# Optimization experiments

Measured on AMD Instinct MI355X. Metric: run time of the kernel, lower is better.

Reference implementation:

```python
import jax, jax.numpy as jnp
import numpy as np
from jax import lax

# dims
B_SZ, H_SZ, W_SZ = 2, 48, 48
D_MODEL = 192
SSM_RATIO = 2.0
D_PROJ = int(SSM_RATIO * D_MODEL)        # 384
C_INNER = 2 * D_PROJ                     # 768 = K * D_IN
K_GRP = 4
D_IN = C_INNER // K_GRP                  # 192 (= d_inner, channel_divide=2)
N_STATE = 16
R_RANK = 12                              # ceil(192/16)


def setup_inputs() -> dict:
    key = jax.random.key(0)
    ks = jax.random.split(key, 12)
    x = jax.random.normal(ks[0], (B_SZ, H_SZ, W_SZ, 2 * D_MODEL), jnp.float32)
    in_proj_w = jax.random.normal(ks[1], (C_INNER, 2 * D_MODEL), jnp.float32) * 0.02
    conv_w = jax.random.normal(ks[2], (C_INNER, 1, 3, 3), jnp.float32) * 0.1
    conv_b = jnp.zeros((C_INNER,), jnp.float32)
    x_proj_weight = jax.random.normal(ks[3], (K_GRP, R_RANK + 2 * N_STATE, D_IN), jnp.float32) * 0.05
    dt_projs_weight = jax.random.normal(ks[4], (K_GRP, D_IN, R_RANK), jnp.float32) * (R_RANK ** -0.5)
    # faithful dt bias init: softplus^{-1}(dt) with dt ~ logU[1e-3, 1e-1]
    dt = jnp.exp(jax.random.uniform(ks[5], (K_GRP, D_IN)) * (np.log(0.1) - np.log(0.001)) + np.log(0.001))
    dt = jnp.clip(dt, 1e-4, None)
    dt_projs_bias = dt + jnp.log(-jnp.expm1(-dt))
    # A_log init: log(arange(1..N)) per channel, K copies merged
    A_logs = jnp.log(jnp.tile(jnp.arange(1, N_STATE + 1, dtype=jnp.float32)[None, :], (K_GRP * D_IN, 1)))
    Ds = jnp.ones((K_GRP * D_IN,), jnp.float32)
    out_norm_w = jnp.ones((C_INNER,), jnp.float32)
    out_norm_b = jnp.zeros((C_INNER,), jnp.float32)
    out_proj_w = jax.random.normal(ks[6], (2 * D_MODEL, C_INNER), jnp.float32) * 0.02
    return dict(x=x, in_proj_w=in_proj_w, conv_w=conv_w, conv_b=conv_b,
                x_proj_weight=x_proj_weight, dt_projs_weight=dt_projs_weight,
                dt_projs_bias=dt_projs_bias, A_logs=A_logs, Ds=Ds,
                out_norm_w=out_norm_w, out_norm_b=out_norm_b, out_proj_w=out_proj_w)


def _ss2d(x, in_proj_w, conv_w, conv_b, x_proj_weight, dt_projs_weight,
          dt_projs_bias, A_logs, Ds, out_norm_w, out_norm_b, out_proj_w):
    B, H, W, _ = x.shape
    C = in_proj_w.shape[0]
    K = x_proj_weight.shape[0]
    d = C // K
    N = A_logs.shape[1]
    R = dt_projs_weight.shape[2]
    L = H * W

    # in_proj (disable_z: no gating split)
    xz = jnp.einsum('bhwc,oc->bhwo', x, in_proj_w)
    xc = xz.transpose(0, 3, 1, 2)  # [B,C,H,W]
    # depthwise 3x3 conv + SiLU
    xc = lax.conv_general_dilated(xc, conv_w, (1, 1), 'SAME', feature_group_count=C)
    xc = xc + conv_b[None, :, None, None]
    xc = xc * jax.nn.sigmoid(xc)

    # CrossScanS: split channels into K groups, each scanned in its own direction
    ch = xc.reshape(B, K, d, H, W)
    f0 = ch[:, 0].reshape(B, d, L)                                        # row-major fwd
    f1 = ch[:, 1].transpose(0, 1, 3, 2).reshape(B, d, L)                  # col-major fwd
    f2 = jnp.flip(ch[:, 2].reshape(B, d, L), -1)                          # row-major rev
    f3 = jnp.flip(ch[:, 3].transpose(0, 1, 3, 2).reshape(B, d, L), -1)    # col-major rev
    xs = jnp.stack([f0, f1, f2, f3], axis=1)  # [B,K,d,L]

    # input-dependent dt/B/C projections
    x_dbl = jnp.einsum('bkdl,kcd->bkcl', xs, x_proj_weight)
    dts, Bs, Cs = jnp.split(x_dbl, [R, R + N], axis=2)  # [B,K,R,L],[B,K,N,L],[B,K,N,L]
    dts = jnp.einsum('bkrl,kdr->bkdl', dts, dt_projs_weight) + dt_projs_bias[None, :, :, None]

    # force_fp32 selective scan with delta_softplus
    u = xs.astype(jnp.float32)
    dts = jax.nn.softplus(dts.astype(jnp.float32))
    Bs = Bs.astype(jnp.float32)
    Cs = Cs.astype(jnp.float32)
    A = -jnp.exp(A_logs.astype(jnp.float32)).reshape(K, d, N)  # [K,d,N]

    def step(h, inp):
        u_t, dt_t, B_t, C_t = inp  # [B,K,d],[B,K,d],[B,K,N],[B,K,N]
        h = h * jnp.exp(dt_t[..., None] * A) + (dt_t * u_t)[..., None] * B_t[:, :, None, :]
        y_t = jnp.einsum('bkdn,bkn->bkd', h, C_t)
        return h, y_t

    inps = (u.transpose(3, 0, 1, 2), dts.transpose(3, 0, 1, 2),
            Bs.transpose(3, 0, 1, 2), Cs.transpose(3, 0, 1, 2))
    h0 = jnp.zeros((B, K, d, N), jnp.float32)
    _, ys = lax.scan(step, h0, inps)          # ys: [L,B,K,d]
    ys = ys.transpose(1, 2, 3, 0)             # [B,K,d,L]
    ys = ys + Ds.astype(jnp.float32).reshape(K, d)[None, :, :, None] * u

    # CrossMergeS: undo each direction, concat channels back
    y0 = ys[:, 0]
    y1 = ys[:, 1].reshape(B, d, W, H).transpose(0, 1, 3, 2).reshape(B, d, L)
    y2 = jnp.flip(ys[:, 2], -1)
    y3 = jnp.flip(ys[:, 3], -1).reshape(B, d, W, H).transpose(0, 1, 3, 2).reshape(B, d, L)
    y = jnp.concatenate([y0, y1, y2, y3], axis=1).reshape(B, C, H, W).transpose(0, 2, 3, 1)

    # out_norm: LayerNorm over channels
    mu = jnp.mean(y, -1, keepdims=True)
    var = jnp.mean(jnp.square(y - mu), -1, keepdims=True)
    y = (y - mu) * lax.rsqrt(var + 1e-5) * out_norm_w + out_norm_b

    out = jnp.einsum('bhwc,oc->bhwo', y.astype(x.dtype), out_proj_w)
    return out


def reference(x, in_proj_w, conv_w, conv_b, x_proj_weight, dt_projs_weight,
              dt_projs_bias, A_logs, Ds, out_norm_w, out_norm_b, out_proj_w):
    return _ss2d(x, in_proj_w, conv_w, conv_b, x_proj_weight, dt_projs_weight,
                 dt_projs_bias, A_logs, Ds, out_norm_w, out_norm_b, out_proj_w)
```

## Files before the change

### kernel.cpp

```cpp
#include <hip/hip_runtime.h>
#include <hip/hip_bf16.h>

#define B_SZ   2
#define H_SZ   48
#define W_SZ   48
#define L_SZ   2304
#define CIN    768
#define KG     4
#define DI     192
#define NS     16
#define RR     12
#define XD     44
#define MTOK   4608
#define CL     16
#define NC     144
#define NXF    (MTOK * 384)
#define NWF    (CIN * 384)

typedef __attribute__((ext_vector_type(8))) short short8;
typedef __attribute__((ext_vector_type(4))) float f32x4;

__device__ inline ushort f2b(float f) {
    uint u = __builtin_bit_cast(uint, f);
    u = (u + 0x7FFF + ((u >> 16) & 1)) >> 16;
    return (ushort)u;
}
__device__ inline float b2f(ushort b) {
    uint u = ((uint)b) << 16;
    return __builtin_bit_cast(float, u);
}
__device__ inline short8 f2b8(float4 a, float4 b) {
    short8 r;
    r[0] = (short)f2b(a.x); r[1] = (short)f2b(a.y);
    r[2] = (short)f2b(a.z); r[3] = (short)f2b(a.w);
    r[4] = (short)f2b(b.x); r[5] = (short)f2b(b.y);
    r[6] = (short)f2b(b.z); r[7] = (short)f2b(b.w);
    return r;
}

__global__ __launch_bounds__(256) void to_bf16_3(
        const float* __restrict__ x, const float* __restrict__ inw,
        const float* __restrict__ outw, ushort* __restrict__ xb,
        ushort* __restrict__ inwb, ushort* __restrict__ outwb) {
    int i4 = (blockIdx.x * 256 + threadIdx.x) * 4;
    const float* src; ushort* dst; int off;
    if (i4 < NXF)             { src = x;    dst = xb;    off = i4; }
    else if (i4 < NXF + NWF)  { src = inw;  dst = inwb;  off = i4 - NXF; }
    else                      { src = outw; dst = outwb; off = i4 - NXF - NWF; }
    float4 v = *(const float4*)&src[off];
    ushort4 u = {f2b(v.x), f2b(v.y), f2b(v.z), f2b(v.w)};
    *(ushort4*)&dst[off] = u;
}

__device__ inline void gridbar(uint* bar, uint nb) {
    __syncthreads();
    if (threadIdx.x == 0) {
        uint g = __hip_atomic_load(&bar[1], __ATOMIC_RELAXED, __HIP_MEMORY_SCOPE_AGENT);
        uint a = __hip_atomic_fetch_add(&bar[0], 1u, __ATOMIC_ACQ_REL, __HIP_MEMORY_SCOPE_AGENT);
        if (a == nb - 1u) {
            __hip_atomic_store(&bar[0], 0u, __ATOMIC_RELAXED, __HIP_MEMORY_SCOPE_AGENT);
            __hip_atomic_store(&bar[1], g + 1u, __ATOMIC_RELEASE, __HIP_MEMORY_SCOPE_AGENT);
        } else {
            while (__hip_atomic_load(&bar[1], __ATOMIC_ACQUIRE, __HIP_MEMORY_SCOPE_AGENT) == g) {
                __builtin_amdgcn_s_sleep(8);
            }
        }
    }
    __syncthreads();
}

template<int TM, int TN, bool ABF, bool BBF, bool CBF>
__global__ __launch_bounds__(256) void gemm_tn(
        const void* __restrict__ Av, const void* __restrict__ Bw,
        void* __restrict__ Cv, int M, int N, int K) {
    __shared__ ushort As[TM][72];
    __shared__ ushort Bs[TN][72];
    constexpr int MF   = TM / 64;
    constexpr int NF   = TN / 16;
    constexpr int ANUM = TM / 32;
    constexpr int BNUM = TN / 32;
    const int tid  = threadIdx.x;
    const int lane = tid & 63;
    const int wave = tid >> 6;
    const int wrow = wave * (MF * 16);
    const int bm = blockIdx.y * TM, bn = blockIdx.x * TN;
    const int frow = lane & 15;
    const int fk   = (lane >> 4) * 8;
    const int orow = (lane >> 4) * 4;

    f32x4 acc[MF][NF] = {};

    for (int k0 = 0; k0 < K; k0 += 64) {
        short8 aval[ANUM];
#pragma unroll
        for (int i = 0; i < ANUM; ++i) {
            int idx = tid + i * 256;
            int row = idx >> 3, q = idx & 7;
            if (ABF) {
                aval[i] = *(const short8*)&((const ushort*)Av)[(size_t)(bm + row) * K + k0 + q * 8];
            } else {
                const float* ap = &((const float*)Av)[(size_t)(bm + row) * K + k0 + q * 8];
                aval[i] = f2b8(*(const float4*)ap, *(const float4*)(ap + 4));
            }
        }
        short8 bval[BNUM];
#pragma unroll
        for (int i = 0; i < BNUM; ++i) {
            int idx = tid + i * 256;
            int row = idx >> 3, q = idx & 7;
            if (BBF) {
                bval[i] = *(const short8*)&((const ushort*)Bw)[(size_t)(bn + row) * K + k0 + q * 8];
            } else {
                const float* bp = &((const float*)Bw)[(size_t)(bn + row) * K + k0 + q * 8];
                bval[i] = f2b8(*(const float4*)bp, *(const float4*)(bp + 4));
            }
        }

        __syncthreads();
#pragma unroll
        for (int i = 0; i < ANUM; ++i) {
            int idx = tid + i * 256;
            *(short8*)&As[idx >> 3][(idx & 7) * 8] = aval[i];
        }
#pragma unroll
        for (int i = 0; i < BNUM; ++i) {
            int idx = tid + i * 256;
            *(short8*)&Bs[idx >> 3][(idx & 7) * 8] = bval[i];
        }
        __syncthreads();

#pragma unroll
        for (int hf = 0; hf < 2; ++hf) {
            short8 af[MF], bf[NF];
#pragma unroll
            for (int mi = 0; mi < MF; ++mi)
                af[mi] = *(const short8*)&As[wrow + mi * 16 + frow][hf * 32 + fk];
#pragma unroll
            for (int ni = 0; ni < NF; ++ni)
                bf[ni] = *(const short8*)&Bs[ni * 16 + frow][hf * 32 + fk];
#pragma unroll
            for (int mi = 0; mi < MF; ++mi)
#pragma unroll
                for (int ni = 0; ni < NF; ++ni)
                    acc[mi][ni] = __builtin_amdgcn_mfma_f32_16x16x32_bf16(
                                      af[mi], bf[ni], acc[mi][ni], 0, 0, 0);
        }
    }

#pragma unroll
    for (int mi = 0; mi < MF; ++mi) {
        int rbase = bm + wrow + mi * 16 + orow;
#pragma unroll
        for (int ni = 0; ni < NF; ++ni) {
            int col = bn + ni * 16 + frow;
#pragma unroll
            for (int r = 0; r < 4; ++r) {
                if (CBF)
                    ((ushort*)Cv)[(size_t)(rbase + r) * N + col] = f2b(acc[mi][ni][r]);
                else
                    ((float*)Cv)[(size_t)(rbase + r) * N + col] = acc[mi][ni][r];
            }
        }
    }
}

__global__ __launch_bounds__(256) void conv_silu_scatter(
        const ushort* __restrict__ xzb, const float* __restrict__ cw,
        const float* __restrict__ cb, ushort* __restrict__ xsb) {
    int g = blockIdx.x * 256 + threadIdx.x;
    int c8 = g % 96;
    int pos = g / 96;
    int w = pos % W_SZ;
    int h = (pos / W_SZ) % H_SZ;
    int b = pos / (W_SZ * H_SZ);
    int c0 = c8 * 8;

    float wt[72];
    const float* cwp = &cw[c0 * 9];
#pragma unroll
    for (int i = 0; i < 18; ++i) {
        float4 v = *(const float4*)(cwp + i * 4);
        wt[i * 4 + 0] = v.x; wt[i * 4 + 1] = v.y;
        wt[i * 4 + 2] = v.z; wt[i * 4 + 3] = v.w;
    }
    float acc[8];
#pragma unroll
    for (int j = 0; j < 8; ++j) acc[j] = cb[c0 + j];

#pragma unroll
    for (int dh = -1; dh <= 1; ++dh) {
        int hh = h + dh;
        if (hh < 0 || hh >= H_SZ) continue;
#pragma unroll
        for (int dw = -1; dw <= 1; ++dw) {
            int ww = w + dw;
            if (ww < 0 || ww >= W_SZ) continue;
            int tap = (dh + 1) * 3 + (dw + 1);
            short8 xv = *(const short8*)&xzb[(size_t)((b * H_SZ + hh) * W_SZ + ww) * CIN + c0];
#pragma unroll
            for (int j = 0; j < 8; ++j)
                acc[j] = fmaf(b2f((ushort)xv[j]), wt[j * 9 + tap], acc[j]);
        }
    }

    float s[8];
#pragma unroll
    for (int j = 0; j < 8; ++j)
        s[j] = acc[j] * __builtin_amdgcn_rcpf(1.f + __expf(-acc[j]));

    int k = c0 / DI, d = c0 % DI;
    int lrow = h * W_SZ + w;
    int lcol = w * H_SZ + h;
    int l;
    if      (k == 0) l = lrow;
    else if (k == 1) l = lcol;
    else if (k == 2) l = L_SZ - 1 - lrow;
    else             l = L_SZ - 1 - lcol;
    float4 lo = {s[0], s[1], s[2], s[3]}, hi = {s[4], s[5], s[6], s[7]};
    *(short8*)&xsb[(size_t)((b * KG + k) * L_SZ + l) * DI + d] = f2b8(lo, hi);
}

__global__ __launch_bounds__(384) void xproj_dt_mfma(
        const ushort* __restrict__ xsb, const float* __restrict__ xpw,
        const float* __restrict__ dtw, const float* __restrict__ dtb,
        float* __restrict__ xdbl, ushort* __restrict__ dts_b) {
    __shared__ ushort Ws[48][200];
    __shared__ ushort Wd[192][40];
    __shared__ ushort dsh[32][40];

    const int tid  = threadIdx.x;
    const int lane = tid & 63;
    const int wave = tid >> 6;
    const int bm = blockIdx.x * 32;
    const int bk = blockIdx.y;
    const int k  = bk & 3;
    const int frow = lane & 15;
    const int fk   = (lane >> 4) * 8;
    const int orow = (lane >> 4) * 4;
    const int rg = wave & 1;
    const int cg = wave >> 1;

#pragma unroll
    for (int i = 0; i < 6; ++i) {
        int idx = tid + i * 384;
        int row = idx / 48, g = idx % 48;
        ushort4 u = {0, 0, 0, 0};
        if (row < XD) {
            float4 v = *(const float4*)&xpw[((size_t)(k * XD) + row) * 192 + g * 4];
            u.x = f2b(v.x); u.y = f2b(v.y); u.z = f2b(v.z); u.w = f2b(v.w);
        }
        *(ushort4*)&Ws[row][g * 4] = u;
    }
#pragma unroll
    for (int i = 0; i < 3; ++i) {
        int idx = tid + i * 384;
        if (idx < 960) {
            float4 z = {0.f, 0.f, 0.f, 0.f};
            *(float4*)&Wd[idx / 5][(idx % 5) * 8] = z;
        } else if (idx < 1120) {
            int j = idx - 960;
            float4 z = {0.f, 0.f, 0.f, 0.f};
            *(float4*)&dsh[j / 5][(j % 5) * 8] = z;
        }
    }
    __syncthreads();

#pragma unroll
    for (int i = 0; i < 6; ++i) {
        int idx = tid + i * 384;
        int row = idx / RR, c = idx % RR;
        Wd[row][c] = f2b(dtw[((size_t)(k * DI) + row) * RR + c]);
    }

    f32x4 acc1 = {};
    const ushort* arow = &xsb[(size_t)(bk * L_SZ + bm + rg * 16 + frow) * DI];
#pragma unroll
    for (int k0 = 0; k0 < 192; k0 += 32) {
        short8 af = *(const short8*)&arow[k0 + fk];
        short8 bv = *(const short8*)&Ws[cg * 16 + frow][k0 + fk];
        acc1 = __builtin_amdgcn_mfma_f32_16x16x32_bf16(af, bv, acc1, 0, 0, 0);
    }

    {
        int col = cg * 16 + frow;
#pragma unroll
        for (int r = 0; r < 4; ++r) {
            float v = acc1[r];
            int row = rg * 16 + orow + r;
            if (col >= RR && col < XD)
                xdbl[(size_t)(bk * L_SZ + bm + row) * XD + col] = v;
            if (cg == 0 && col < RR)
                dsh[row][col] = f2b(v);
        }
    }
    __syncthreads();

#pragma unroll
    for (int t = 0; t < 2; ++t) {
        int d = (wave * 2 + t) * 16 + frow;
        short8 bv = *(const short8*)&Wd[d][fk];
        float bias = dtb[k * DI + d];
#pragma unroll
        for (int rg2 = 0; rg2 < 2; ++rg2) {
            short8 af2 = *(const short8*)&dsh[rg2 * 16 + frow][fk];
            f32x4 a2 = {};
            a2 = __builtin_amdgcn_mfma_f32_16x16x32_bf16(af2, bv, a2, 0, 0, 0);
#pragma unroll
            for (int r = 0; r < 4; ++r) {
                float a = a2[r] + bias;
                float sp = fmaxf(a, 0.f) + __logf(1.f + __expf(-fabsf(a)));
                dts_b[(size_t)(bk * L_SZ + bm + rg2 * 16 + orow + r) * DI + d] = f2b(sp);
            }
        }
    }
}

__global__ __launch_bounds__(192, 4) void scan_fused(
        const ushort* __restrict__ dts_b, const ushort* __restrict__ xsb,
        const float* __restrict__ xdbl, const float* __restrict__ A_logs,
        float* __restrict__ Ebuf, float* __restrict__ Sbuf,
        float* __restrict__ Pbuf, float* __restrict__ Hstart,
        const float* __restrict__ Ds, ushort* __restrict__ ypre_b,
        const float* __restrict__ lnw, const float* __restrict__ lnb,
        ushort* __restrict__ ynrm_b, uint* __restrict__ bar) {
    const int blk = blockIdx.x;
    const int bk = blk / NC, ch = blk % NC;
    const int d = threadIdx.x, k = bk % KG, b = bk / KG;
    const int l0 = ch * CL;

    __shared__ float bsh[CL][NS];
    __shared__ float csh[CL][NS];
    __shared__ float red[2][3];
    for (int t = threadIdx.x; t < CL * NS; t += 192) {
        int l = t / NS, n = t % NS;
        const float* row = &xdbl[(size_t)(bk * L_SZ + l0 + l) * XD];
        bsh[l][n] = row[RR + n];
        csh[l][n] = row[RR + NS + n];
    }
    __syncthreads();

    {
        float Aa[NS], S[NS];
        const float* ar = &A_logs[(size_t)(k * DI + d) * NS];
        bool fast = true;
#pragma unroll
        for (int n = 0; n < NS; ++n) {
            Aa[n] = -__expf(ar[n]);
            S[n] = 0.f;
            fast = fast && (fabsf(Aa[n] + (float)(n + 1)) < 1e-4f * (n + 1));
        }
        float* sp = &Sbuf[(size_t)((bk * NC + ch) * DI + d) * NS];
        if (fast) {
            float P = 1.f;
#pragma unroll
            for (int l = 0; l < CL; ++l) {
                float dt = b2f(dts_b[(size_t)(bk * L_SZ + l0 + l) * DI + d]);
                float u  = b2f(xsb [(size_t)(bk * L_SZ + l0 + l) * DI + d]);
                float du = dt * u;
                float4 b0 = *(const float4*)&bsh[l][0];
                float4 b1 = *(const float4*)&bsh[l][4];
                float4 b2 = *(const float4*)&bsh[l][8];
                float4 b3 = *(const float4*)&bsh[l][12];
                float Bv[NS] = {b0.x,b0.y,b0.z,b0.w, b1.x,b1.y,b1.z,b1.w,
                                b2.x,b2.y,b2.z,b2.w, b3.x,b3.y,b3.z,b3.w};
                float e1 = __expf(-dt);
                P *= e1;
                float e = e1;
                S[0] = fmaf(S[0], e, du * Bv[0]);
#pragma unroll
                for (int n = 1; n < NS; ++n) {
                    e *= e1;
                    S[n] = fmaf(S[n], e, du * Bv[n]);
                }
            }
            Pbuf[(size_t)(bk * NC + ch) * DI + d] = P;
#pragma unroll
            for (int q = 0; q < 4; ++q) {
                float4 v = {S[q*4], S[q*4+1], S[q*4+2], S[q*4+3]};
                *(float4*)&sp[q * 4] = v;
            }
        } else {
            float E[NS];
#pragma unroll
            for (int n = 0; n < NS; ++n) E[n] = 1.f;
#pragma unroll 8
            for (int l = 0; l < CL; ++l) {
                float dt = b2f(dts_b[(size_t)(bk * L_SZ + l0 + l) * DI + d]);
                float u  = b2f(xsb [(size_t)(bk * L_SZ + l0 + l) * DI + d]);
                float du = dt * u;
                float4 b0 = *(const float4*)&bsh[l][0];
                float4 b1 = *(const float4*)&bsh[l][4];
                float4 b2 = *(const float4*)&bsh[l][8];
                float4 b3 = *(const float4*)&bsh[l][12];
                float Bv[NS] = {b0.x,b0.y,b0.z,b0.w, b1.x,b1.y,b1.z,b1.w,
                                b2.x,b2.y,b2.z,b2.w, b3.x,b3.y,b3.z,b3.w};
#pragma unroll
                for (int n = 0; n < NS; ++n) {
                    float e = __expf(dt * Aa[n]);
                    E[n] *= e;
                    S[n] = fmaf(S[n], e, du * Bv[n]);
                }
            }
            Pbuf[(size_t)(bk * NC + ch) * DI + d] = -1.f;
            float* ep = &Ebuf[(size_t)((bk * NC + ch) * DI + d) * NS];
#pragma unroll
            for (int q = 0; q < 4; ++q) {
                float4 ve = {E[q*4], E[q*4+1], E[q*4+2], E[q*4+3]};
                float4 vs = {S[q*4], S[q*4+1], S[q*4+2], S[q*4+3]};
                *(float4*)&ep[q * 4] = ve;
                *(float4*)&sp[q * 4] = vs;
            }
        }
    }

    gridbar(bar, gridDim.x);

    {
        constexpr int P = 8;
        int t = blk * 192 + threadIdx.x;
        if (t < 8 * DI * 4) {
            int bkB = t / (DI * 4);
            int dn = (t % (DI * 4)) * 4;
            int dB = dn >> 4;
            int n0 = dn & 15;
            const size_t stride = (size_t)DI * NS;
            size_t off = (size_t)(bkB * NC) * stride + dn;
            const float* pb = &Pbuf[(size_t)(bkB * NC) * DI + dB];

            float4 h = {0.f, 0.f, 0.f, 0.f};
            bool fastu = (pb[0] >= 0.f);

            if (fastu) {
                float  pA[P], pB2[P];
                float4 sA[P], sB[P];
                size_t offL = off;
                int    cP   = 0;
#pragma unroll
                for (int j = 0; j < P; ++j) {
                    pA[j] = pb[(size_t)(cP + j) * DI];
                    sA[j] = *(const float4*)&Sbuf[offL + (size_t)j * stride];
                }
                offL += (size_t)P * stride; cP += P;

                for (int c = 0; c < NC; c += 2 * P) {
#pragma unroll
                    for (int j = 0; j < P; ++j) {
                        pB2[j] = pb[(size_t)(cP + j) * DI];
                        sB[j] = *(const float4*)&Sbuf[offL + (size_t)j * stride];
                    }
                    offL += (size_t)P * stride; cP += P;

#pragma unroll
                    for (int j = 0; j < P; ++j) {
                        *(float4*)&Hstart[off + (size_t)j * stride] = h;
                        float Pv = pA[j];
                        float P2 = Pv * Pv, P3 = P2 * Pv;
                        float P4 = P2 * P2, P8 = P4 * P4;
                        float base = Pv * ((n0 & 4) ? P4 : 1.f) * ((n0 & 8) ? P8 : 1.f);
                        h.x = fmaf(base,      h.x, sA[j].x);
                        h.y = fmaf(base * Pv, h.y, sA[j].y);
                        h.z = fmaf(base * P2, h.z, sA[j].z);
                        h.w = fmaf(base * P3, h.w, sA[j].w);
                    }
                    off += (size_t)P * stride;

                    if (c + 2 * P < NC) {
#pragma unroll
                        for (int j = 0; j < P; ++j) {
                            pA[j] = pb[(size_t)(cP + j) * DI];
                            sA[j] = *(const float4*)&Sbuf[offL + (size_t)j * stride];
                        }
                    }
                    offL += (size_t)P * stride; cP += P;

#pragma unroll
                    for (int j = 0; j < P; ++j) {
                        *(float4*)&Hstart[off + (size_t)j * stride] = h;
                        float Pv = pB2[j];
                        float P2 = Pv * Pv, P3 = P2 * Pv;
                        float P4 = P2 * P2, P8 = P4 * P4;
                        float base = Pv * ((n0 & 4) ? P4 : 1.f) * ((n0 & 8) ? P8 : 1.f);
                        h.x = fmaf(base,      h.x, sB[j].x);
                        h.y = fmaf(base * Pv, h.y, sB[j].y);
                        h.z = fmaf(base * P2, h.z, sB[j].z);
                        h.w = fmaf(base * P3, h.w, sB[j].w);
                    }
                    off += (size_t)P * stride;
                }
            } else {
                float4 eA[P], sA[P], eB[P], sB[P];
                size_t offL = off;
#pragma unroll
                for (int j = 0; j < P; ++j) {
                    eA[j] = *(const float4*)&Ebuf[offL + (size_t)j * stride];
                    sA[j] = *(const float4*)&Sbuf[offL + (size_t)j * stride];
                }
                offL += (size_t)P * stride;

                for (int c = 0; c < NC; c += 2 * P) {
#pragma unroll
                    for (int j = 0; j < P; ++j) {
                        eB[j] = *(const float4*)&Ebuf[offL + (size_t)j * stride];
                        sB[j] = *(const float4*)&Sbuf[offL + (size_t)j * stride];
                    }
                    offL += (size_t)P * stride;

#pragma unroll
                    for (int j = 0; j < P; ++j) {
                        *(float4*)&Hstart[off + (size_t)j * stride] = h;
                        h.x = fmaf(eA[j].x, h.x, sA[j].x);
                        h.y = fmaf(eA[j].y, h.y, sA[j].y);
                        h.z = fmaf(eA[j].z, h.z, sA[j].z);
                        h.w = fmaf(eA[j].w, h.w, sA[j].w);
                    }
                    off += (size_t)P * stride;

                    if (c + 2 * P < NC) {
#pragma unroll
                        for (int j = 0; j < P; ++j) {
                            eA[j] = *(const float4*)&Ebuf[offL + (size_t)j * stride];
                            sA[j] = *(const float4*)&Sbuf[offL + (size_t)j * stride];
                        }
                    }
                    offL += (size_t)P * stride;

#pragma unroll
                    for (int j = 0; j < P; ++j) {
                        *(float4*)&Hstart[off + (size_t)j * stride] = h;
                        h.x = fmaf(eB[j].x, h.x, sB[j].x);
                        h.y = fmaf(eB[j].y, h.y, sB[j].y);
                        h.z = fmaf(eB[j].z, h.z, sB[j].z);
                        h.w = fmaf(eB[j].w, h.w, sB[j].w);
                    }
                    off += (size_t)P * stride;
                }
            }
        }
    }

    gridbar(bar, gridDim.x);

    {
        float Aa[NS], h[NS];
        const float* ar = &A_logs[(size_t)(k * DI + d) * NS];
        const float* hp = &Hstart[(size_t)((bk * NC + ch) * DI + d) * NS];
        bool fast = true;
#pragma unroll
        for (int n = 0; n < NS; ++n) {
            Aa[n] = -__expf(ar[n]);
            h[n] = hp[n];
            fast = fast && (fabsf(Aa[n] + (float)(n + 1)) < 1e-4f * (n + 1));
        }
        float Dd = Ds[k * DI + d];

#pragma unroll 8
        for (int l = 0; l < CL; ++l) {
            float dt = b2f(dts_b[(size_t)(bk * L_SZ + l0 + l) * DI + d]);
            float u  = b2f(xsb [(size_t)(bk * L_SZ + l0 + l) * DI + d]);
            float du = dt * u;
            float4 b0 = *(const float4*)&bsh[l][0];
            float4 b1 = *(const float4*)&bsh[l][4];
            float4 b2 = *(const float4*)&bsh[l][8];
            float4 b3 = *(const float4*)&bsh[l][12];
            float Bv[NS] = {b0.x,b0.y,b0.z,b0.w, b1.x,b1.y,b1.z,b1.w,
                            b2.x,b2.y,b2.z,b2.w, b3.x,b3.y,b3.z,b3.w};
            float4 c0 = *(const float4*)&csh[l][0];
            float4 c1 = *(const float4*)&csh[l][4];
            float4 c2 = *(const float4*)&csh[l][8];
            float4 c3 = *(const float4*)&csh[l][12];
            float Cv[NS] = {c0.x,c0.y,c0.z,c0.w, c1.x,c1.y,c1.z,c1.w,
                            c2.x,c2.y,c2.z,c2.w, c3.x,c3.y,c3.z,c3.w};
            float p[NS];
            if (fast) {
                float e1 = __expf(-dt);
                float e = e1;
                h[0] = fmaf(h[0], e, du * Bv[0]);
                p[0] = h[0] * Cv[0];
#pragma unroll
                for (int n = 1; n < NS; ++n) {
                    e *= e1;
                    h[n] = fmaf(h[n], e, du * Bv[n]);
                    p[n] = h[n] * Cv[n];
                }
            } else {
#pragma unroll
                for (int n = 0; n < NS; ++n) {
                    float e = __expf(dt * Aa[n]);
                    h[n] = fmaf(h[n], e, du * Bv[n]);
                    p[n] = h[n] * Cv[n];
                }
            }
#pragma unroll
            for (int s = 8; s >= 1; s >>= 1)
#pragma unroll
                for (int n = 0; n < 8; ++n)
                    if (n < s) p[n] = p[n] + p[n + s];
            float y = fmaf(Dd, u, p[0]);

            int lg = l0 + l;
            int pos;
            if      (k == 0) pos = lg;
            else if (k == 1) pos = (lg % H_SZ) * W_SZ + (lg / H_SZ);
            else if (k == 2) pos = L_SZ - 1 - lg;
            else { int j = L_SZ - 1 - lg; pos = (j % H_SZ) * W_SZ + (j / H_SZ); }
            ypre_b[(size_t)(b * L_SZ + pos) * CIN + k * DI + d] = f2b(y);
        }
    }

    gridbar(bar, gridDim.x);

    {
        int lane = threadIdx.x & 63, wv = threadIdx.x >> 6;
        int i4 = threadIdx.x * 4;
        float4 w4 = *(const float4*)&lnw[i4];
        float4 g4 = *(const float4*)&lnb[i4];
        for (int j = 0; j < 4; ++j) {
            int tok = blk * 4 + j;
            ushort4 rv = *(const ushort4*)&ypre_b[(size_t)tok * CIN + i4];
            float v0 = b2f(rv.x), v1 = b2f(rv.y), v2 = b2f(rv.z), v3 = b2f(rv.w);
            float s1 = v0 + v1 + v2 + v3;
            float s2 = v0*v0 + v1*v1 + v2*v2 + v3*v3;
#pragma unroll
            for (int off = 32; off >= 1; off >>= 1) {
                s1 += __shfl_xor(s1, off, 64);
                s2 += __shfl_xor(s2, off, 64);
            }
            if (lane == 0) { red[0][wv] = s1; red[1][wv] = s2; }
            __syncthreads();
            float ts1 = red[0][0] + red[0][1] + red[0][2];
            float ts2 = red[1][0] + red[1][1] + red[1][2];
            float mu = ts1 * (1.f / CIN);
            float rstd = rsqrtf(ts2 * (1.f / CIN) - mu * mu + 1e-5f);
            ushort4 o;
            o.x = f2b((v0 - mu) * rstd * w4.x + g4.x);
            o.y = f2b((v1 - mu) * rstd * w4.y + g4.y);
            o.z = f2b((v2 - mu) * rstd * w4.z + g4.z);
            o.w = f2b((v3 - mu) * rstd * w4.w + g4.w);
            *(ushort4*)&ynrm_b[(size_t)tok * CIN + i4] = o;
            __syncthreads();
        }
    }
}

__global__ __launch_bounds__(192) void scan_passA(
        const ushort* __restrict__ dts_b, const ushort* __restrict__ xsb,
        const float* __restrict__ xdbl, const float* __restrict__ A_logs,
        float* __restrict__ Ebuf, float* __restrict__ Sbuf,
        float* __restrict__ Pbuf) {
    int blk = blockIdx.x;
    int bk = blk / NC, ch = blk % NC;
    int d = threadIdx.x, k = bk % KG;
    int l0 = ch * CL;

    __shared__ float bsh[CL][NS];
    for (int t = threadIdx.x; t < CL * NS; t += 192) {
        int l = t / NS, n = t % NS;
        bsh[l][n] = xdbl[(size_t)(bk * L_SZ + l0 + l) * XD + RR + n];
    }
    __syncthreads();

    float Aa[NS], S[NS];
    const float* ar = &A_logs[(size_t)(k * DI + d) * NS];
    bool fast = true;
#pragma unroll
    for (int n = 0; n < NS; ++n) {
        Aa[n] = -__expf(ar[n]);
        S[n] = 0.f;
        fast = fast && (fabsf(Aa[n] + (float)(n + 1)) < 1e-4f * (n + 1));
    }

    float* sp = &Sbuf[(size_t)((bk * NC + ch) * DI + d) * NS];
    if (fast) {
        float P = 1.f;
#pragma unroll
        for (int l = 0; l < CL; ++l) {
            float dt = b2f(dts_b[(size_t)(bk * L_SZ + l0 + l) * DI + d]);
            float u  = b2f(xsb [(size_t)(bk * L_SZ + l0 + l) * DI + d]);
            float du = dt * u;
            float4 b0 = *(const float4*)&bsh[l][0];
            float4 b1 = *(const float4*)&bsh[l][4];
            float4 b2 = *(const float4*)&bsh[l][8];
            float4 b3 = *(const float4*)&bsh[l][12];
            float Bv[NS] = {b0.x,b0.y,b0.z,b0.w, b1.x,b1.y,b1.z,b1.w,
                            b2.x,b2.y,b2.z,b2.w, b3.x,b3.y,b3.z,b3.w};
            float e1 = __expf(-dt);
            P *= e1;
            float e = e1;
            S[0] = fmaf(S[0], e, du * Bv[0]);
#pragma unroll
            for (int n = 1; n < NS; ++n) {
                e *= e1;
                S[n] = fmaf(S[n], e, du * Bv[n]);
            }
        }
        Pbuf[(size_t)(bk * NC + ch) * DI + d] = P;
#pragma unroll
        for (int q = 0; q < 4; ++q) {
            float4 v = {S[q*4], S[q*4+1], S[q*4+2], S[q*4+3]};
            *(float4*)&sp[q * 4] = v;
        }
    } else {
        float E[NS];
#pragma unroll
        for (int n = 0; n < NS; ++n) E[n] = 1.f;
#pragma unroll 8
        for (int l = 0; l < CL; ++l) {
            float dt = b2f(dts_b[(size_t)(bk * L_SZ + l0 + l) * DI + d]);
            float u  = b2f(xsb [(size_t)(bk * L_SZ + l0 + l) * DI + d]);
            float du = dt * u;
            float4 b0 = *(const float4*)&bsh[l][0];
            float4 b1 = *(const float4*)&bsh[l][4];
            float4 b2 = *(const float4*)&bsh[l][8];
            float4 b3 = *(const float4*)&bsh[l][12];
            float Bv[NS] = {b0.x,b0.y,b0.z,b0.w, b1.x,b1.y,b1.z,b1.w,
                            b2.x,b2.y,b2.z,b2.w, b3.x,b3.y,b3.z,b3.w};
#pragma unroll
            for (int n = 0; n < NS; ++n) {
                float e = __expf(dt * Aa[n]);
                E[n] *= e;
                S[n] = fmaf(S[n], e, du * Bv[n]);
            }
        }
        Pbuf[(size_t)(bk * NC + ch) * DI + d] = -1.f;
        float* ep = &Ebuf[(size_t)((bk * NC + ch) * DI + d) * NS];
#pragma unroll
        for (int q = 0; q < 4; ++q) {
            float4 ve = {E[q*4], E[q*4+1], E[q*4+2], E[q*4+3]};
            float4 vs = {S[q*4], S[q*4+1], S[q*4+2], S[q*4+3]};
            *(float4*)&ep[q * 4] = ve;
            *(float4*)&sp[q * 4] = vs;
        }
    }
}

__global__ __launch_bounds__(64) void scan_passB(
        const float* __restrict__ Ebuf, const float* __restrict__ Sbuf,
        const float* __restrict__ Pbuf, float* __restrict__ Hstart) {
    constexpr int P = 8;
    int t = blockIdx.x * 64 + threadIdx.x;
    int bk = t / (DI * 4);
    int dn = (t % (DI * 4)) * 4;
    int d  = dn >> 4;
    int n0 = dn & 15;
    const size_t stride = (size_t)DI * NS;
    size_t off  = (size_t)(bk * NC) * stride + dn;
    const float* pb = &Pbuf[(size_t)(bk * NC) * DI + d];

    float4 h = {0.f, 0.f, 0.f, 0.f};
    bool fastu = (pb[0] >= 0.f);

    if (fastu) {
        float  pA[P], pB[P];
        float4 sA[P], sB[P];
        size_t offL = off;
        int    cP   = 0;
#pragma unroll
        for (int j = 0; j < P; ++j) {
            pA[j] = pb[(size_t)(cP + j) * DI];
            sA[j] = *(const float4*)&Sbuf[offL + (size_t)j * stride];
        }
        offL += (size_t)P * stride; cP += P;

        for (int c = 0; c < NC; c += 2 * P) {
#pragma unroll
            for (int j = 0; j < P; ++j) {
                pB[j] = pb[(size_t)(cP + j) * DI];
                sB[j] = *(const float4*)&Sbuf[offL + (size_t)j * stride];
            }
            offL += (size_t)P * stride; cP += P;

#pragma unroll
            for (int j = 0; j < P; ++j) {
                *(float4*)&Hstart[off + (size_t)j * stride] = h;
                float Pv = pA[j];
                float P2 = Pv * Pv, P3 = P2 * Pv;
                float P4 = P2 * P2, P8 = P4 * P4;
                float base = Pv * ((n0 & 4) ? P4 : 1.f) * ((n0 & 8) ? P8 : 1.f);
                h.x = fmaf(base,      h.x, sA[j].x);
                h.y = fmaf(base * Pv, h.y, sA[j].y);
                h.z = fmaf(base * P2, h.z, sA[j].z);
                h.w = fmaf(base * P3, h.w, sA[j].w);
            }
            off += (size_t)P * stride;

            if (c + 2 * P < NC) {
#pragma unroll
                for (int j = 0; j < P; ++j) {
                    pA[j] = pb[(size_t)(cP + j) * DI];
                    sA[j] = *(const float4*)&Sbuf[offL + (size_t)j * stride];
                }
            }
            offL += (size_t)P * stride; cP += P;

#pragma unroll
            for (int j = 0; j < P; ++j) {
                *(float4*)&Hstart[off + (size_t)j * stride] = h;
                float Pv = pB[j];
                float P2 = Pv * Pv, P3 = P2 * Pv;
                float P4 = P2 * P2, P8 = P4 * P4;
                float base = Pv * ((n0 & 4) ? P4 : 1.f) * ((n0 & 8) ? P8 : 1.f);
                h.x = fmaf(base,      h.x, sB[j].x);
                h.y = fmaf(base * Pv, h.y, sB[j].y);
                h.z = fmaf(base * P2, h.z, sB[j].z);
                h.w = fmaf(base * P3, h.w, sB[j].w);
            }
            off += (size_t)P * stride;
        }
    } else {
        float4 eA[P], sA[P], eB[P], sB[P];
        size_t offL = off;
#pragma unroll
        for (int j = 0; j < P; ++j) {
            eA[j] = *(const float4*)&Ebuf[offL + (size_t)j * stride];
            sA[j] = *(const float4*)&Sbuf[offL + (size_t)j * stride];
        }
        offL += (size_t)P * stride;

        for (int c = 0; c < NC; c += 2 * P) {
#pragma unroll
            for (int j = 0; j < P; ++j) {
                eB[j] = *(const float4*)&Ebuf[offL + (size_t)j * stride];
                sB[j] = *(const float4*)&Sbuf[offL + (size_t)j * stride];
            }
            offL += (size_t)P * stride;

#pragma unroll
            for (int j = 0; j < P; ++j) {
                *(float4*)&Hstart[off + (size_t)j * stride] = h;
                h.x = fmaf(eA[j].x, h.x, sA[j].x);
                h.y = fmaf(eA[j].y, h.y, sA[j].y);
                h.z = fmaf(eA[j].z, h.z, sA[j].z);
                h.w = fmaf(eA[j].w, h.w, sA[j].w);
            }
            off += (size_t)P * stride;

            if (c + 2 * P < NC) {
#pragma unroll
                for (int j = 0; j < P; ++j) {
                    eA[j] = *(const float4*)&Ebuf[offL + (size_t)j * stride];
                    sA[j] = *(const float4*)&Sbuf[offL + (size_t)j * stride];
                }
            }
            offL += (size_t)P * stride;

#pragma unroll
            for (int j = 0; j < P; ++j) {
                *(float4*)&Hstart[off + (size_t)j * stride] = h;
                h.x = fmaf(eB[j].x, h.x, sB[j].x);
                h.y = fmaf(eB[j].y, h.y, sB[j].y);
                h.z = fmaf(eB[j].z, h.z, sB[j].z);
                h.w = fmaf(eB[j].w, h.w, sB[j].w);
            }
            off += (size_t)P * stride;
        }
    }
}

__global__ __launch_bounds__(192) void scan_passC(
        const ushort* __restrict__ dts_b, const ushort* __restrict__ xsb,
        const float* __restrict__ xdbl, const float* __restrict__ A_logs,
        const float* __restrict__ Hstart, const float* __restrict__ Ds,
        ushort* __restrict__ ypre_b) {
    int blk = blockIdx.x;
    int bk = blk / NC, ch = blk % NC;
    int d = threadIdx.x, k = bk % KG, b = bk / KG;
    int l0 = ch * CL;

    __shared__ float bsh[CL][NS];
    __shared__ float csh[CL][NS];
    for (int t = threadIdx.x; t < CL * NS; t += 192) {
        int l = t / NS, n = t % NS;
        const float* row = &xdbl[(size_t)(bk * L_SZ + l0 + l) * XD];
        bsh[l][n] = row[RR + n];
        csh[l][n] = row[RR + NS + n];
    }
    __syncthreads();

    float Aa[NS], h[NS];
    const float* ar = &A_logs[(size_t)(k * DI + d) * NS];
    const float* hp = &Hstart[(size_t)((bk * NC + ch) * DI + d) * NS];
    bool fast = true;
#pragma unroll
    for (int n = 0; n < NS; ++n) {
        Aa[n] = -__expf(ar[n]);
        h[n] = hp[n];
        fast = fast && (fabsf(Aa[n] + (float)(n + 1)) < 1e-4f * (n + 1));
    }
    float Dd = Ds[k * DI + d];

#pragma unroll 8
    for (int l = 0; l < CL; ++l) {
        float dt = b2f(dts_b[(size_t)(bk * L_SZ + l0 + l) * DI + d]);
        float u  = b2f(xsb [(size_t)(bk * L_SZ + l0 + l) * DI + d]);
        float du = dt * u;
        float4 b0 = *(const float4*)&bsh[l][0];
        float4 b1 = *(const float4*)&bsh[l][4];
        float4 b2 = *(const float4*)&bsh[l][8];
        float4 b3 = *(const float4*)&bsh[l][12];
        float Bv[NS] = {b0.x,b0.y,b0.z,b0.w, b1.x,b1.y,b1.z,b1.w,
                        b2.x,b2.y,b2.z,b2.w, b3.x,b3.y,b3.z,b3.w};
        float4 c0 = *(const float4*)&csh[l][0];
        float4 c1 = *(const float4*)&csh[l][4];
        float4 c2 = *(const float4*)&csh[l][8];
        float4 c3 = *(const float4*)&csh[l][12];
        float Cv[NS] = {c0.x,c0.y,c0.z,c0.w, c1.x,c1.y,c1.z,c1.w,
                        c2.x,c2.y,c2.z,c2.w, c3.x,c3.y,c3.z,c3.w};
        float p[NS];
        if (fast) {
            float e1 = __expf(-dt);
            float e = e1;
            h[0] = fmaf(h[0], e, du * Bv[0]);
            p[0] = h[0] * Cv[0];
#pragma unroll
            for (int n = 1; n < NS; ++n) {
                e *= e1;
                h[n] = fmaf(h[n], e, du * Bv[n]);
                p[n] = h[n] * Cv[n];
            }
        } else {
#pragma unroll
            for (int n = 0; n < NS; ++n) {
                float e = __expf(dt * Aa[n]);
                h[n] = fmaf(h[n], e, du * Bv[n]);
                p[n] = h[n] * Cv[n];
            }
        }
#pragma unroll
        for (int s = 8; s >= 1; s >>= 1)
#pragma unroll
            for (int n = 0; n < 8; ++n)
                if (n < s) p[n] = p[n] + p[n + s];
        float y = fmaf(Dd, u, p[0]);

        int lg = l0 + l;
        int pos;
        if      (k == 0) pos = lg;
        else if (k == 1) pos = (lg % H_SZ) * W_SZ + (lg / H_SZ);
        else if (k == 2) pos = L_SZ - 1 - lg;
        else { int j = L_SZ - 1 - lg; pos = (j % H_SZ) * W_SZ + (j / H_SZ); }
        ypre_b[(size_t)(b * L_SZ + pos) * CIN + k * DI + d] = f2b(y);
    }
}

__global__ __launch_bounds__(256) void layernorm_bf16(
        const ushort* __restrict__ y, ushort* __restrict__ yb,
        const float* __restrict__ w, const float* __restrict__ bg) {
    int wave = threadIdx.x >> 6, lane = threadIdx.x & 63;
    int tok = blockIdx.x * 4 + wave;
    const ushort* row = &y[(size_t)tok * CIN];
    ushort* rowo = &yb[(size_t)tok * CIN];
    float v[12];
    float s = 0.f;
#pragma unroll
    for (int i = 0; i < 12; ++i) { v[i] = b2f(row[lane + i * 64]); s += v[i]; }
#pragma unroll
    for (int off = 32; off >= 1; off >>= 1) s += __shfl_xor(s, off, 64);
    float mu = s * (1.f / CIN);
    float s2 = 0.f;
#pragma unroll
    for (int i = 0; i < 12; ++i) { float t = v[i] - mu; s2 += t * t; }
#pragma unroll
    for (int off = 32; off >= 1; off >>= 1) s2 += __shfl_xor(s2, off, 64);
    float rstd = rsqrtf(s2 * (1.f / CIN) + 1e-5f);
#pragma unroll
    for (int i = 0; i < 12; ++i)
        rowo[lane + i * 64] =
            f2b((v[i] - mu) * rstd * w[lane + i * 64] + bg[lane + i * 64]);
}

extern "C" void kernel_launch(void* const* d_in, const int* in_sizes, int n_in,
                              void* d_out, int out_size, void* d_ws, size_t ws_size,
                              hipStream_t stream) {
    const float* x    = (const float*)d_in[0];
    const float* inw  = (const float*)d_in[1];
    const float* cw   = (const float*)d_in[2];
    const float* cb   = (const float*)d_in[3];
    const float* xpw  = (const float*)d_in[4];
    const float* dtw  = (const float*)d_in[5];
    const float* dtb  = (const float*)d_in[6];
    const float* alog = (const float*)d_in[7];
    const float* Dsp  = (const float*)d_in[8];
    const float* lnw  = (const float*)d_in[9];
    const float* lnb  = (const float*)d_in[10];
    const float* outw = (const float*)d_in[11];
    float* out = (float*)d_out;

    float* ws = (float*)d_ws;
    const size_t SZ_BIG = (size_t)MTOK * CIN;
    const size_t SCAN_SL = (size_t)8 * NC * DI * NS;
    float* xz    = ws;
    float* xsbf  = xz  + SZ_BIG;
    float* dts   = xsbf + SZ_BIG / 2;
    float* xdbl  = dts + SZ_BIG;
    float* Ebuf  = xdbl + (size_t)8 * L_SZ * XD;
    float* Sbuf  = Ebuf + SCAN_SL;
    float* Hst   = Sbuf + SCAN_SL;
    float* Pbuf  = Hst + SCAN_SL;
    ushort* xb   = (ushort*)(Pbuf + (size_t)8 * NC * DI);
    ushort* inwb = xb + NXF;
    ushort* outwb= inwb + NWF;
    uint*  bar   = (uint*)(outwb + NWF);
    ushort* xzb    = (ushort*)xz;
    ushort* xsb    = (ushort*)xsbf;
    ushort* dtsb   = (ushort*)dts;
    ushort* ypre_b = (ushort*)xz;
    ushort* ynrm_b = (ushort*)dts;

    to_bf16_3<<<(NXF + 2 * NWF) / 1024, 256, 0, stream>>>(x, inw, outw, xb, inwb, outwb);
    gemm_tn<64, 64, true, true, true><<<dim3(CIN / 64, MTOK / 64), 256, 0, stream>>>(
        xb, inwb, xzb, MTOK, CIN, 384);
    conv_silu_scatter<<<(B_SZ * H_SZ * W_SZ * 96) / 256, 256, 0, stream>>>(xzb, cw, cb, xsb);
    xproj_dt_mfma<<<dim3(L_SZ / 32, 8), 384, 0, stream>>>(xsb, xpw, dtw, dtb, xdbl, dtsb);

    int maxb = 0;
    hipError_t oe = hipOccupancyMaxActiveBlocksPerMultiprocessor(
        &maxb, scan_fused, 192, 0);
    if (oe == hipSuccess && maxb * 256 >= 8 * NC) {
        hipMemsetAsync(bar, 0, 2 * sizeof(uint), stream);
        scan_fused<<<8 * NC, 192, 0, stream>>>(
            dtsb, xsb, xdbl, alog, Ebuf, Sbuf, Pbuf, Hst, Dsp, ypre_b,
            lnw, lnb, ynrm_b, bar);
    } else {
        scan_passA<<<8 * NC, 192, 0, stream>>>(dtsb, xsb, xdbl, alog, Ebuf, Sbuf, Pbuf);
        scan_passB<<<(8 * DI * 4) / 64, 64, 0, stream>>>(Ebuf, Sbuf, Pbuf, Hst);
        scan_passC<<<8 * NC, 192, 0, stream>>>(dtsb, xsb, xdbl, alog, Hst, Dsp, ypre_b);
        layernorm_bf16<<<MTOK / 4, 256, 0, stream>>>(ypre_b, ynrm_b, lnw, lnb);
    }
    gemm_tn<64, 32, true, true, false><<<dim3(384 / 32, MTOK / 64), 256, 0, stream>>>(
        ynrm_b, outwb, out, MTOK, 384, CIN);
}
```

Baseline: 177.1 us.

## Fuse bf16 conversion into in_proj GEMM and out_proj into persistent scan

Merges the fp32-to-bf16 conversion kernel with the in_proj GEMM using a grid-wide barrier, and appends the out_proj GEMM to the persistent scan_fused kernel after another grid barrier, tiling it 48x32 per block. This removes two kernel launches and their inter-kernel gaps. In exchange it relies on all 864 GEMM blocks being co-resident (checked only as at least 4 blocks per CU), adds shared memory to the scan kernel that may lower its occupancy, and uses small output tiles for the out_proj.

```diff
diff --git a/kernel.cpp b/kernel.cpp
--- a/kernel.cpp
+++ b/kernel.cpp
@@ -38,6 +38,97 @@
     return r;
 }
 
+__device__ inline void gridbar(uint* bar, uint nb) {
+    __syncthreads();
+    if (threadIdx.x == 0) {
+        uint g = __hip_atomic_load(&bar[1], __ATOMIC_RELAXED, __HIP_MEMORY_SCOPE_AGENT);
+        uint a = __hip_atomic_fetch_add(&bar[0], 1u, __ATOMIC_ACQ_REL, __HIP_MEMORY_SCOPE_AGENT);
+        if (a == nb - 1u) {
+            __hip_atomic_store(&bar[0], 0u, __ATOMIC_RELAXED, __HIP_MEMORY_SCOPE_AGENT);
+            __hip_atomic_store(&bar[1], g + 1u, __ATOMIC_RELEASE, __HIP_MEMORY_SCOPE_AGENT);
+        } else {
+            while (__hip_atomic_load(&bar[1], __ATOMIC_ACQUIRE, __HIP_MEMORY_SCOPE_AGENT) == g) {
+                __builtin_amdgcn_s_sleep(8);
+            }
+        }
+    }
+    __syncthreads();
+}
+
+__global__ __launch_bounds__(256) void gemm1_fused(
+        const float* __restrict__ x, const float* __restrict__ inw,
+        const float* __restrict__ outw, ushort* __restrict__ xb,
+        ushort* __restrict__ inwb, ushort* __restrict__ outwb,
+        ushort* __restrict__ Cv, uint* __restrict__ bar) {
+    constexpr int N = CIN, K = 384;
+    __shared__ ushort As[64][72];
+    __shared__ ushort Bs[64][72];
+    const int tid  = threadIdx.x;
+    const int flatb = blockIdx.y * gridDim.x + blockIdx.x;
+
+    for (int u = flatb * 256 + tid; u < (NXF + 2 * NWF) / 4; u += 864 * 256) {
+        int i4 = u * 4;
+        const float* src; ushort* dst; int off;
+        if (i4 < NXF)            { src = x;    dst = xb;    off = i4; }
+        else if (i4 < NXF + NWF) { src = inw;  dst = inwb;  off = i4 - NXF; }
+        else                     { src = outw; dst = outwb; off = i4 - NXF - NWF; }
+        float4 v = *(const float4*)&src[off];
+        ushort4 uu = {f2b(v.x), f2b(v.y), f2b(v.z), f2b(v.w)};
+        *(ushort4*)&dst[off] = uu;
+    }
+    gridbar(bar, 864);
+
+    const int lane = tid & 63;
+    const int wave = tid >> 6;
+    const int wrow = wave * 16;
+    const int bm = blockIdx.y * 64, bn = blockIdx.x * 64;
+    const int frow = lane & 15;
+    const int fk   = (lane >> 4) * 8;
+    const int orow = (lane >> 4) * 4;
+
+    f32x4 acc[4] = {};
+
+    for (int k0 = 0; k0 < K; k0 += 64) {
+        short8 aval[2], bval[2];
+#pragma unroll
+        for (int i = 0; i < 2; ++i) {
+            int idx = tid + i * 256;
+            int row = idx >> 3, q = idx & 7;
+            aval[i] = *(const short8*)&xb[(size_t)(bm + row) * K + k0 + q * 8];
+            bval[i] = *(const short8*)&inwb[(size_t)(bn + row) * K + k0 + q * 8];
+        }
+        __syncthreads();
+#pragma unroll
+        for (int i = 0; i < 2; ++i) {
+            int idx = tid + i * 256;
+            *(short8*)&As[idx >> 3][(idx & 7) * 8] = aval[i];
+            *(short8*)&Bs[idx >> 3][(idx & 7) * 8] = bval[i];
+        }
+        __syncthreads();
+
+#pragma unroll
+        for (int hf = 0; hf < 2; ++hf) {
+            short8 af = *(const short8*)&As[wrow + frow][hf * 32 + fk];
+            short8 bf[4];
+#pragma unroll
+            for (int ni = 0; ni < 4; ++ni)
+                bf[ni] = *(const short8*)&Bs[ni * 16 + frow][hf * 32 + fk];
+#pragma unroll
+            for (int ni = 0; ni < 4; ++ni)
+                acc[ni] = __builtin_amdgcn_mfma_f32_16x16x32_bf16(af, bf[ni], acc[ni], 0, 0, 0);
+        }
+    }
+
+    int rbase = bm + wrow + orow;
+#pragma unroll
+    for (int ni = 0; ni < 4; ++ni) {
+        int col = bn + ni * 16 + frow;
+#pragma unroll
+        for (int r = 0; r < 4; ++r)
+            Cv[(size_t)(rbase + r) * N + col] = f2b(acc[ni][r]);
+    }
+}
+
 __global__ __launch_bounds__(256) void to_bf16_3(
         const float* __restrict__ x, const float* __restrict__ inw,
         const float* __restrict__ outw, ushort* __restrict__ xb,
@@ -52,26 +143,9 @@
     *(ushort4*)&dst[off] = u;
 }
 
-__device__ inline void gridbar(uint* bar, uint nb) {
-    __syncthreads();
-    if (threadIdx.x == 0) {
-        uint g = __hip_atomic_load(&bar[1], __ATOMIC_RELAXED, __HIP_MEMORY_SCOPE_AGENT);
-        uint a = __hip_atomic_fetch_add(&bar[0], 1u, __ATOMIC_ACQ_REL, __HIP_MEMORY_SCOPE_AGENT);
-        if (a == nb - 1u) {
-            __hip_atomic_store(&bar[0], 0u, __ATOMIC_RELAXED, __HIP_MEMORY_SCOPE_AGENT);
-            __hip_atomic_store(&bar[1], g + 1u, __ATOMIC_RELEASE, __HIP_MEMORY_SCOPE_AGENT);
-        } else {
-            while (__hip_atomic_load(&bar[1], __ATOMIC_ACQUIRE, __HIP_MEMORY_SCOPE_AGENT) == g) {
-                __builtin_amdgcn_s_sleep(8);
-            }
-        }
-    }
-    __syncthreads();
-}
-
-template<int TM, int TN, bool ABF, bool BBF, bool CBF>
+template<int TM, int TN, bool CBF>
 __global__ __launch_bounds__(256) void gemm_tn(
-        const void* __restrict__ Av, const void* __restrict__ Bw,
+        const ushort* __restrict__ Av, const ushort* __restrict__ Bw,
         void* __restrict__ Cv, int M, int N, int K) {
     __shared__ ushort As[TM][72];
     __shared__ ushort Bs[TN][72];
@@ -91,31 +165,17 @@
     f32x4 acc[MF][NF] = {};
 
     for (int k0 = 0; k0 < K; k0 += 64) {
-        short8 aval[ANUM];
+        short8 aval[ANUM], bval[BNUM];
 #pragma unroll
         for (int i = 0; i < ANUM; ++i) {
             int idx = tid + i * 256;
-            int row = idx >> 3, q = idx & 7;
-            if (ABF) {
-                aval[i] = *(const short8*)&((const ushort*)Av)[(size_t)(bm + row) * K + k0 + q * 8];
-            } else {
-                const float* ap = &((const float*)Av)[(size_t)(bm + row) * K + k0 + q * 8];
-                aval[i] = f2b8(*(const float4*)ap, *(const float4*)(ap + 4));
-            }
-        }
-        short8 bval[BNUM];
+            aval[i] = *(const short8*)&Av[(size_t)(bm + (idx >> 3)) * K + k0 + (idx & 7) * 8];
+        }
 #pragma unroll
         for (int i = 0; i < BNUM; ++i) {
             int idx = tid + i * 256;
-            int row = idx >> 3, q = idx & 7;
-            if (BBF) {
-                bval[i] = *(const short8*)&((const ushort*)Bw)[(size_t)(bn + row) * K + k0 + q * 8];
-            } else {
-                const float* bp = &((const float*)Bw)[(size_t)(bn + row) * K + k0 + q * 8];
-                bval[i] = f2b8(*(const float4*)bp, *(const float4*)(bp + 4));
-            }
-        }
-
+            bval[i] = *(const short8*)&Bw[(size_t)(bn + (idx >> 3)) * K + k0 + (idx & 7) * 8];
+        }
         __syncthreads();
 #pragma unroll
         for (int i = 0; i < ANUM; ++i) {
@@ -322,7 +382,8 @@
         float* __restrict__ Pbuf, float* __restrict__ Hstart,
         const float* __restrict__ Ds, ushort* __restrict__ ypre_b,
         const float* __restrict__ lnw, const float* __restrict__ lnb,
-        ushort* __restrict__ ynrm_b, uint* __restrict__ bar) {
+        ushort* __restrict__ ynrm_b, const ushort* __restrict__ outwb,
+        float* __restrict__ out, uint* __restrict__ bar) {
     const int blk = blockIdx.x;
     const int bk = blk / NC, ch = blk % NC;
     const int d = threadIdx.x, k = bk % KG, b = bk / KG;
@@ -331,6 +392,8 @@
     __shared__ float bsh[CL][NS];
     __shared__ float csh[CL][NS];
     __shared__ float red[2][3];
+    __shared__ ushort As2[48][72];
+    __shared__ ushort Bs2[32][72];
     for (int t = threadIdx.x; t < CL * NS; t += 192) {
         int l = t / NS, n = t % NS;
         const float* row = &xdbl[(size_t)(bk * L_SZ + l0 + l) * XD];
@@ -640,6 +703,65 @@
             __syncthreads();
         }
     }
+
+    gridbar(bar, gridDim.x);
+
+    {
+        const int em = blk / 12, en = blk % 12;
+        const int bm2 = em * 48, bn2 = en * 32;
+        const int lane2 = threadIdx.x & 63;
+        const int wv = threadIdx.x >> 6;
+        const int frow2 = lane2 & 15;
+        const int fk2   = (lane2 >> 4) * 8;
+        const int orow2 = (lane2 >> 4) * 4;
+        f32x4 acc[2] = {};
+
+        for (int k0 = 0; k0 < CIN; k0 += 64) {
+            short8 aval[2];
+#pragma unroll
+            for (int i = 0; i < 2; ++i) {
+                int idx = threadIdx.x + i * 192;
+                aval[i] = *(const short8*)&ynrm_b[(size_t)(bm2 + (idx >> 3)) * CIN + k0 + (idx & 7) * 8];
+            }
+            short8 bval0 = *(const short8*)&outwb[(size_t)(bn2 + (threadIdx.x >> 3)) * CIN + k0 + (threadIdx.x & 7) * 8];
+            short8 bval1;
+            if (threadIdx.x < 64) {
+                int idx = threadIdx.x + 192;
+                bval1 = *(const short8*)&outwb[(size_t)(bn2 + (idx >> 3)) * CIN + k0 + (idx & 7) * 8];
+            }
+            __syncthreads();
+#pragma unroll
+            for (int i = 0; i < 2; ++i) {
+                int idx = threadIdx.x + i * 192;
+                *(short8*)&As2[idx >> 3][(idx & 7) * 8] = aval[i];
+            }
+            *(short8*)&Bs2[threadIdx.x >> 3][(threadIdx.x & 7) * 8] = bval0;
+            if (threadIdx.x < 64) {
+                int idx = threadIdx.x + 192;
+                *(short8*)&Bs2[idx >> 3][(idx & 7) * 8] = bval1;
+            }
+            __syncthreads();
+
+#pragma unroll
+            for (int hf = 0; hf < 2; ++hf) {
+                short8 af = *(const short8*)&As2[wv * 16 + frow2][hf * 32 + fk2];
+#pragma unroll
+                for (int ni = 0; ni < 2; ++ni) {
+                    short8 bf = *(const short8*)&Bs2[ni * 16 + frow2][hf * 32 + fk2];
+                    acc[ni] = __builtin_amdgcn_mfma_f32_16x16x32_bf16(af, bf, acc[ni], 0, 0, 0);
+                }
+            }
+        }
+
+        int rbase = bm2 + wv * 16 + orow2;
+#pragma unroll
+        for (int ni = 0; ni < 2; ++ni) {
+            int col = bn2 + ni * 16 + frow2;
+#pragma unroll
+            for (int r = 0; r < 4; ++r)
+                out[(size_t)(rbase + r) * 384 + col] = acc[ni][r];
+        }
+    }
 }
 
 __global__ __launch_bounds__(192) void scan_passA(
@@ -1006,26 +1128,35 @@
     ushort* ypre_b = (ushort*)xz;
     ushort* ynrm_b = (ushort*)dts;
 
-    to_bf16_3<<<(NXF + 2 * NWF) / 1024, 256, 0, stream>>>(x, inw, outw, xb, inwb, outwb);
-    gemm_tn<64, 64, true, true, true><<<dim3(CIN / 64, MTOK / 64), 256, 0, stream>>>(
-        xb, inwb, xzb, MTOK, CIN, 384);
+    int maxb1 = 0, maxbS = 0;
+    hipError_t e1 = hipOccupancyMaxActiveBlocksPerMultiprocessor(&maxb1, gemm1_fused, 256, 0);
+    hipError_t eS = hipOccupancyMaxActiveBlocksPerMultiprocessor(&maxbS, scan_fused, 192, 0);
+    bool f1 = (e1 == hipSuccess && maxb1 >= 4);
+    bool fS = (eS == hipSuccess && maxbS * 256 >= 8 * NC);
+
+    hipMemsetAsync(bar, 0, 4 * sizeof(uint), stream);
+
+    if (f1) {
+        gemm1_fused<<<dim3(CIN / 64, MTOK / 64), 256, 0, stream>>>(
+            x, inw, outw, xb, inwb, outwb, xzb, bar + 2);
+    } else {
+        to_bf16_3<<<(NXF + 2 * NWF) / 1024, 256, 0, stream>>>(x, inw, outw, xb, inwb, outwb);
+        gemm_tn<64, 64, true><<<dim3(CIN / 64, MTOK / 64), 256, 0, stream>>>(
+            xb, inwb, xzb, MTOK, CIN, 384);
+    }
     conv_silu_scatter<<<(B_SZ * H_SZ * W_SZ * 96) / 256, 256, 0, stream>>>(xzb, cw, cb, xsb);
     xproj_dt_mfma<<<dim3(L_SZ / 32, 8), 384, 0, stream>>>(xsb, xpw, dtw, dtb, xdbl, dtsb);
 
-    int maxb = 0;
-    hipError_t oe = hipOccupancyMaxActiveBlocksPerMultiprocessor(
-        &maxb, scan_fused, 192, 0);
-    if (oe == hipSuccess && maxb * 256 >= 8 * NC) {
-        hipMemsetAsync(bar, 0, 2 * sizeof(uint), stream);
+    if (fS) {
         scan_fused<<<8 * NC, 192, 0, stream>>>(
             dtsb, xsb, xdbl, alog, Ebuf, Sbuf, Pbuf, Hst, Dsp, ypre_b,
-            lnw, lnb, ynrm_b, bar);
+            lnw, lnb, ynrm_b, outwb, out, bar);
     } else {
         scan_passA<<<8 * NC, 192, 0, stream>>>(dtsb, xsb, xdbl, alog, Ebuf, Sbuf, Pbuf);
         scan_passB<<<(8 * DI * 4) / 64, 64, 0, stream>>>(Ebuf, Sbuf, Pbuf, Hst);
         scan_passC<<<8 * NC, 192, 0, stream>>>(dtsb, xsb, xdbl, alog, Hst, Dsp, ypre_b);
         layernorm_bf16<<<MTOK / 4, 256, 0, stream>>>(ypre_b, ynrm_b, lnw, lnb);
-    }
-    gemm_tn<64, 32, true, true, false><<<dim3(384 / 32, MTOK / 64), 256, 0, stream>>>(
-        ynrm_b, outwb, out, MTOK, 384, CIN);
-}
+        gemm_tn<64, 32, false><<<dim3(384 / 32, MTOK / 64), 256, 0, stream>>>(
+            ynrm_b, outwb, out, MTOK, 384, CIN);
+    }
+}
```

Measured after the change: 177.4 us. Within noise of the previous version (+0.2%).
